# Kernel optimization log

Measured on AMD Instinct MI355X. Metric: run time of the kernel, lower is better.

Reference implementation:

```python
import jax, jax.numpy as jnp
import numpy as np

N_NODES = 50000
N_EDGES = 400000
DIMS = [128, 1024, 512, 256, 64, 1]  # ConvGraphNet layer widths


def setup_inputs() -> dict:
    key = jax.random.key(0)
    ks = jax.random.split(key, 2 + 2 * 5)
    inp = {}
    inp["x"] = jax.random.normal(ks[0], (N_NODES, DIMS[0]), dtype=jnp.float32)
    inp["edge_index"] = jax.random.randint(ks[1], (2, N_EDGES), 0, N_NODES, dtype=jnp.int32)
    for i in range(5):
        fan_in, fan_out = DIMS[i], DIMS[i + 1]
        scale = (1.0 / np.sqrt(fan_in)).astype(np.float32)
        inp[f"W{i+1}"] = jax.random.normal(ks[2 + 2 * i], (fan_in, fan_out), dtype=jnp.float32) * scale
        inp[f"b{i+1}"] = jax.random.normal(ks[3 + 2 * i], (fan_out,), dtype=jnp.float32) * 0.01
    return inp


def _gcn_forward(x, edge_index, params):
    # PyG GCNConv: add self-loops, symmetric deg^{-1/2} normalization,
    # h = x @ W, out[dst] += norm * h[src], + bias. ReLU after each layer.
    src, dst = edge_index[0], edge_index[1]
    loop = jnp.arange(N_NODES, dtype=src.dtype)
    src_f = jnp.concatenate([src, loop])  # [E + N]
    dst_f = jnp.concatenate([dst, loop])
    deg = jax.ops.segment_sum(jnp.ones_like(src_f, dtype=x.dtype), dst_f, num_segments=N_NODES)
    dinv = jnp.where(deg > 0, jax.lax.rsqrt(jnp.maximum(deg, 1e-12)), 0.0).astype(x.dtype)
    norm = (dinv[src_f] * dinv[dst_f])[:, None]  # [E + N, 1]
    for W, b in params:
        h = x @ W                      # [N, F_out] dense GEMM (small)
        msg = h[src_f] * norm          # gather + scale  [E+N, F_out]
        agg = jax.ops.segment_sum(msg, dst_f, num_segments=N_NODES)  # scatter-add
        x = jax.nn.relu(agg + b)
    return x


def reference(x, edge_index, W1, b1, W2, b2, W3, b3, W4, b4, W5, b5):
    params = [(W1, b1), (W2, b2), (W3, b3), (W4, b4), (W5, b5)]
    return _gcn_forward(x, edge_index, params)
```

## Files before the change

### kernel.cpp

```cpp
#include <hip/hip_runtime.h>
#include <hip/hip_bf16.h>

#define N_NODES_DIM0 128

typedef unsigned short u16;
typedef unsigned int u32;
typedef __attribute__((ext_vector_type(8))) short short8;
typedef __attribute__((ext_vector_type(4))) float f32x4;

__device__ __forceinline__ float bf2f(u16 h) { return __uint_as_float((u32)h << 16); }
__device__ __forceinline__ u16 f2bf(float f) {
    u32 u = __float_as_uint(f);
    u32 r = (u + 0x7FFFu + ((u >> 16) & 1u)) >> 16;
    return (u16)r;
}

__device__ __forceinline__ void gl2lds16(const u16* g, u16* lds_base) {
    __builtin_amdgcn_global_load_lds(
        (const __attribute__((address_space(1))) u32*)g,
        (__attribute__((address_space(3))) u32*)lds_base, 16, 0, 0);
}


__global__ void zero_int_kernel(int* p, int n) {
    int i = blockIdx.x * blockDim.x + threadIdx.x;
    if (i < n) p[i] = 0;
}

__global__ void hist_kernel(const int* __restrict__ dst, int* __restrict__ cnt, int e) {
    int i = blockIdx.x * blockDim.x + threadIdx.x;
    if (i < e) atomicAdd(&cnt[dst[i]], 1);
}

__global__ void alloc_kernel(const int* __restrict__ cnt, int* __restrict__ row_start,
                             float* __restrict__ dinv, int* __restrict__ cursor, int n) {
    int i = blockIdx.x * blockDim.x + threadIdx.x;
    int lane = threadIdx.x & 63;
    int v = (i < n) ? cnt[i] : 0;
    int s = v;
#pragma unroll
    for (int off = 1; off < 64; off <<= 1) {
        int x = __shfl_up(s, off, 64);
        if (lane >= off) s += x;
    }
    int total = __shfl(s, 63, 64);
    int base = 0;
    if (lane == 0) base = atomicAdd(cursor, total);
    base = __shfl(base, 0, 64);
    if (i < n) {
        row_start[i] = base + s - v;
        dinv[i] = rsqrtf((float)v + 1.0f);
    }
}

__global__ void fill_kernel(const int* __restrict__ src, const int* __restrict__ dst,
                            int* __restrict__ row_start, int* __restrict__ csr_src, int e) {
    int i = blockIdx.x * blockDim.x + threadIdx.x;
    if (i < e) {
        int d = dst[i];
        int pos = atomicAdd(&row_start[d], 1);
        csr_src[pos] = src[i];
    }
}

__global__ __launch_bounds__(256) void wtrans_kernel(
    const float* __restrict__ W0, const float* __restrict__ W1,
    const float* __restrict__ W2, const float* __restrict__ W3, u16* __restrict__ Wt) {
    __shared__ float tile[32][33];
    int bid = blockIdx.x;
    const float* W; u16* out; int K, F, kb, nb;
    if (bid < 128)      { W = W0; out = Wt;          K = 128;  F = 1024; kb = bid & 3;  nb = bid >> 2; }
    else if (bid < 640) { int l = bid - 128; W = W1; out = Wt + 131072; K = 1024; F = 512; kb = l & 31; nb = l >> 5; }
    else if (bid < 768) { int l = bid - 640; W = W2; out = Wt + 655360; K = 512;  F = 256; kb = l & 15; nb = l >> 4; }
    else                { int l = bid - 768; W = W3; out = Wt + 786432; K = 256;  F = 64;  kb = l & 7;  nb = l >> 3; }
    int k0 = kb * 32, n0 = nb * 32;
    int tx = threadIdx.x & 31, ty = threadIdx.x >> 5;
#pragma unroll
    for (int i = 0; i < 4; ++i) {
        int k = ty + i * 8;
        tile[k][tx] = W[(size_t)(k0 + k) * F + n0 + tx];
    }
    __syncthreads();
#pragma unroll
    for (int i = 0; i < 4; ++i) {
        int n = ty + i * 8;
        out[(size_t)(n0 + n) * K + k0 + tx] = f2bf(tile[tx][n]);
    }
}

__global__ void scale_cast_kernel(const float* __restrict__ x, const float* __restrict__ dinv,
                                  u16* __restrict__ Y, int N) {
    int gid = blockIdx.x * blockDim.x + threadIdx.x;
    int node = gid >> 5;
    int c4 = (gid & 31) * 4;
    if (node >= N) return;
    float dv = dinv[node];
    float4 v = *reinterpret_cast<const float4*>(x + (size_t)node * 128 + c4);
    ushort4 r;
    r.x = f2bf(dv * v.x); r.y = f2bf(dv * v.y);
    r.z = f2bf(dv * v.z); r.w = f2bf(dv * v.w);
    *reinterpret_cast<ushort4*>(Y + (size_t)node * 128 + c4) = r;
}

__device__ __forceinline__ void add8(float* acc, const u16* p) {
    short8 v = *reinterpret_cast<const short8*>(p);
#pragma unroll
    for (int w = 0; w < 8; ++w) acc[w] += bf2f((u16)v[w]);
}
__device__ __forceinline__ void add8v(float* acc, short8 v) {
#pragma unroll
    for (int w = 0; w < 8; ++w) acc[w] += bf2f((u16)v[w]);
}

__global__ void agg_pre_kernel(const int* __restrict__ row_end, const int* __restrict__ cnt,
                               const int* __restrict__ csr_src,
                               const u16* __restrict__ Y, const float* __restrict__ dinv,
                               u16* __restrict__ Z, int N) {
    int gid = blockIdx.x * blockDim.x + threadIdx.x;
    int node = gid >> 4;
    int ch = (gid & 15) * 8;
    if (node >= N) return;
    float acc[8] = {};
    add8(acc, Y + (size_t)node * 128 + ch);
    int end = row_end[node], beg = end - cnt[node];
    int e = beg;
    for (; e + 4 <= end; e += 4) {
        int s0 = csr_src[e], s1 = csr_src[e + 1], s2 = csr_src[e + 2], s3 = csr_src[e + 3];
        short8 v0 = *reinterpret_cast<const short8*>(Y + (size_t)s0 * 128 + ch);
        short8 v1 = *reinterpret_cast<const short8*>(Y + (size_t)s1 * 128 + ch);
        short8 v2 = *reinterpret_cast<const short8*>(Y + (size_t)s2 * 128 + ch);
        short8 v3 = *reinterpret_cast<const short8*>(Y + (size_t)s3 * 128 + ch);
        add8v(acc, v0); add8v(acc, v1); add8v(acc, v2); add8v(acc, v3);
    }
    for (; e < end; ++e) add8(acc, Y + (size_t)csr_src[e] * 128 + ch);
    float dv = dinv[node];
    short8 r;
#pragma unroll
    for (int w = 0; w < 8; ++w) r[w] = (short)f2bf(dv * acc[w]);
    *reinterpret_cast<short8*>(Z + (size_t)node * 128 + ch) = r;
}

template <int BN, int EPI>
__global__ __launch_bounds__(256) void gemm_mfma_kernel(
    const u16* __restrict__ X, const u16* __restrict__ Wt,
    const float* __restrict__ dinv, const float* __restrict__ bias,
    u16* __restrict__ Out, int N, int K, int F, int lgnx) {
    constexpr int BM = 128, BK = 64;
    constexpr int RA = (BM * 8) / 256;
    constexpr int RB = (BN * 8) / 256;
    __shared__ u16 As[BM * BK];
    __shared__ u16 Bs[BN * BK];

    const int t = threadIdx.x;
    const int wave = t >> 6;
    const int lane = t & 63;
    const int m16 = lane & 15;
    const int quad = lane >> 4;

    const int id = blockIdx.x;
    const int wi = id & ((8 << lgnx) - 1);
    const int g  = id >> (3 + lgnx);
    const int rb = g * 8 + (wi & 7);
    const int cb = wi >> 3;
    const int row0 = rb * BM;
    const int col0 = cb * BN;
    if (row0 >= N) return;

    constexpr int WN = BN / 2;
    constexpr int NI = 4;
    constexpr int NJ = WN / 16;
    const int wm = (wave >> 1) * 64;
    const int wn = (wave & 1) * WN;

    const u16* aSrc[RA];
    u16* aDst[RA];
#pragma unroll
    for (int rr = 0; rr < RA; ++rr) {
        int c = rr * 256 + t;
        int r = c >> 3;
        int q = (c ^ r) & 7;
        int grow = row0 + r;
        if (grow >= N) grow = 0;
        aSrc[rr] = X + (size_t)grow * K + q * 8;
        aDst[rr] = &As[(size_t)(rr * 256 + wave * 64) * 8];
    }
    const u16* bSrc[RB];
    u16* bDst[RB];
#pragma unroll
    for (int rr = 0; rr < RB; ++rr) {
        int c = rr * 256 + t;
        int r = c >> 3;
        int q = (c ^ r) & 7;
        bSrc[rr] = Wt + (size_t)(col0 + r) * K + q * 8;
        bDst[rr] = &Bs[(size_t)(rr * 256 + wave * 64) * 8];
    }

    u32 aOff[NI][2], bOff[NJ][2];
#pragma unroll
    for (int i = 0; i < NI; ++i)
#pragma unroll
        for (int h = 0; h < 2; ++h) {
            int row = wm + i * 16 + m16;
            int qg = h * 4 + quad;
            aOff[i][h] = (u32)(((row << 3) | ((qg ^ row) & 7)) * 16);
        }
#pragma unroll
    for (int j = 0; j < NJ; ++j)
#pragma unroll
        for (int h = 0; h < 2; ++h) {
            int row = wn + j * 16 + m16;
            int qg = h * 4 + quad;
            bOff[j][h] = (u32)(((row << 3) | ((qg ^ row) & 7)) * 16);
        }
    const char* AsB = reinterpret_cast<const char*>(As);
    const char* BsB = reinterpret_cast<const char*>(Bs);

    f32x4 acc[NI][NJ] = {};

    for (int k0 = 0; k0 < K; k0 += BK) {
#pragma unroll
        for (int rr = 0; rr < RA; ++rr) {
            gl2lds16(aSrc[rr], aDst[rr]);
            aSrc[rr] += BK;
        }
#pragma unroll
        for (int rr = 0; rr < RB; ++rr) {
            gl2lds16(bSrc[rr], bDst[rr]);
            bSrc[rr] += BK;
        }
        __syncthreads();

#pragma unroll
        for (int h = 0; h < 2; ++h) {
            short8 af[NI], bf[NJ];
#pragma unroll
            for (int i = 0; i < NI; ++i)
                af[i] = *reinterpret_cast<const short8*>(AsB + aOff[i][h]);
#pragma unroll
            for (int j = 0; j < NJ; ++j)
                bf[j] = *reinterpret_cast<const short8*>(BsB + bOff[j][h]);
#pragma unroll
            for (int i = 0; i < NI; ++i)
#pragma unroll
                for (int j = 0; j < NJ; ++j)
                    acc[i][j] = __builtin_amdgcn_mfma_f32_16x16x32_bf16(af[i], bf[j], acc[i][j], 0, 0, 0);
        }
        __syncthreads();
    }

#pragma unroll
    for (int i = 0; i < NI; ++i) {
#pragma unroll
        for (int r = 0; r < 4; ++r) {
            int grow = row0 + wm + i * 16 + quad * 4 + r;
            if (grow >= N) continue;
            float dv = (EPI == 0) ? dinv[grow] : 0.f;
#pragma unroll
            for (int j = 0; j < NJ; ++j) {
                int gcol = col0 + wn + j * 16 + m16;
                float v = acc[i][j][r];
                if (EPI == 0) v = dv * v;
                else          v = fmaxf(v + bias[gcol], 0.f);
                Out[(size_t)grow * F + gcol] = f2bf(v);
            }
        }
    }
}

__global__ void agg_post_kernel(const int* __restrict__ row_end, const int* __restrict__ cnt,
                                const int* __restrict__ csr_src,
                                const u16* __restrict__ Gc, const float* __restrict__ dinv,
                                const float* __restrict__ bias, u16* __restrict__ XO,
                                int N, int F, int lgG) {
    int gid = blockIdx.x * blockDim.x + threadIdx.x;
    int node = gid >> lgG;
    int ch = (gid & ((1 << lgG) - 1)) * 8;
    if (node >= N) return;
    float acc[8] = {};
    add8(acc, Gc + (size_t)node * F + ch);
    int end = row_end[node], beg = end - cnt[node];
    int e = beg;
    for (; e + 4 <= end; e += 4) {
        int s0 = csr_src[e], s1 = csr_src[e + 1], s2 = csr_src[e + 2], s3 = csr_src[e + 3];
        short8 v0 = *reinterpret_cast<const short8*>(Gc + (size_t)s0 * F + ch);
        short8 v1 = *reinterpret_cast<const short8*>(Gc + (size_t)s1 * F + ch);
        short8 v2 = *reinterpret_cast<const short8*>(Gc + (size_t)s2 * F + ch);
        short8 v3 = *reinterpret_cast<const short8*>(Gc + (size_t)s3 * F + ch);
        add8v(acc, v0); add8v(acc, v1); add8v(acc, v2); add8v(acc, v3);
    }
    for (; e < end; ++e) add8(acc, Gc + (size_t)csr_src[e] * F + ch);
    float dv = dinv[node];
    short8 r;
#pragma unroll
    for (int w = 0; w < 8; ++w)
        r[w] = (short)f2bf(fmaxf(fmaf(dv, acc[w], bias[ch + w]), 0.f));
    *reinterpret_cast<short8*>(XO + (size_t)node * F + ch) = r;
}

__global__ void layer5_dot_kernel(const u16* __restrict__ X, const float* __restrict__ W5,
                                  const float* __restrict__ dinv, float* __restrict__ g5, int N) {
    int gtid = blockIdx.x * blockDim.x + threadIdx.x;
    int node = gtid >> 6;
    int lane = threadIdx.x & 63;
    if (node >= N) return;
    float v = bf2f(X[(size_t)node * 64 + lane]) * W5[lane];
#pragma unroll
    for (int off = 32; off > 0; off >>= 1) v += __shfl_down(v, off, 64);
    if (lane == 0) g5[node] = dinv[node] * v;
}

__global__ void agg5_kernel(const int* __restrict__ row_end, const int* __restrict__ cnt,
                            const int* __restrict__ csr_src,
                            const float* __restrict__ g5, const float* __restrict__ dinv,
                            const float* __restrict__ b5, float* __restrict__ out, int N) {
    int i = blockIdx.x * blockDim.x + threadIdx.x;
    if (i >= N) return;
    float acc = g5[i];
    int end = row_end[i], e = end - cnt[i];
    for (; e + 4 <= end; e += 4) {
        float a = g5[csr_src[e]];
        float b = g5[csr_src[e + 1]];
        float c = g5[csr_src[e + 2]];
        float d = g5[csr_src[e + 3]];
        acc += (a + b) + (c + d);
    }
    for (; e < end; ++e) acc += g5[csr_src[e]];
    out[i] = fmaxf(fmaf(dinv[i], acc, b5[0]), 0.f);
}


static inline size_t align_up(size_t x) { return (x + 255) & ~(size_t)255; }
static inline int round_up8(int x) { return (x + 7) & ~7; }

extern "C" void kernel_launch(void* const* d_in, const int* in_sizes, int n_in,
                              void* d_out, int out_size, void* d_ws, size_t ws_size,
                              hipStream_t stream) {
    const float* x  = (const float*)d_in[0];
    const int*   ei = (const int*)d_in[1];
    const int E = in_sizes[1] / 2;
    const int N = in_sizes[0] / N_NODES_DIM0;
    const int* src = ei;
    const int* dst = ei + E;

    const float* W[5] = {(const float*)d_in[2], (const float*)d_in[4], (const float*)d_in[6],
                         (const float*)d_in[8], (const float*)d_in[10]};
    const float* B[5] = {(const float*)d_in[3], (const float*)d_in[5], (const float*)d_in[7],
                         (const float*)d_in[9], (const float*)d_in[11]};

    const int Ks[4] = {128, 1024, 512, 256};
    const int Fs[4] = {1024, 512, 256, 64};

    char* w = (char*)d_ws;
    size_t off = 0;
    float* dinv    = (float*)(w + off); off += align_up((size_t)N * 4);
    float* g5      = (float*)(w + off); off += align_up((size_t)N * 4);
    int*   cnt     = (int*)(w + off);   off += align_up((size_t)(N + 1) * 4);
    int*   rstart  = (int*)(w + off);   off += align_up((size_t)N * 4);
    int*   csr_src = (int*)(w + off);   off += align_up((size_t)E * 4);
    u16* WtBase = (u16*)(w + off);
    u16* Wt[4];
    {
        size_t cum = 0;
        for (int l = 0; l < 4; ++l) {
            Wt[l] = WtBase + cum;
            cum += (size_t)Ks[l] * Fs[l];
        }
        off += align_up(cum * 2);
    }
    char* REG = w + off;               off += align_up((size_t)N * 512 * 2);
    u16* Y  = (u16*)REG;
    u16* Z  = (u16*)(REG + align_up((size_t)N * 128 * 2));
    u16* Gc = (u16*)REG;
    u16* XA = (u16*)(w + off);         off += align_up((size_t)N * 1024 * 2);
    u16* XB = (u16*)(w + off);         off += align_up((size_t)N * 512 * 2);
    (void)ws_size;

    zero_int_kernel<<<(N + 1 + 255) / 256, 256, 0, stream>>>(cnt, N + 1);
    hist_kernel<<<(E + 255) / 256, 256, 0, stream>>>(dst, cnt, E);
    alloc_kernel<<<(N + 255) / 256, 256, 0, stream>>>(cnt, rstart, dinv, &cnt[N], N);
    fill_kernel<<<(E + 255) / 256, 256, 0, stream>>>(src, dst, rstart, csr_src, E);

    wtrans_kernel<<<784, 256, 0, stream>>>(W[0], W[1], W[2], W[3], WtBase);

    const int ny = (N + 127) / 128;
    const int ny8 = round_up8(ny);

    scale_cast_kernel<<<(N * 32 + 255) / 256, 256, 0, stream>>>(x, dinv, Y, N);
    agg_pre_kernel<<<(N * 16 + 255) / 256, 256, 0, stream>>>(rstart, cnt, csr_src, Y, dinv, Z, N);
    {
        gemm_mfma_kernel<128, 1><<<ny8 * 8, 256, 0, stream>>>(Z, Wt[0], dinv, B[0], XA,
                                                              N, 128, 1024, 3);
    }

    u16* Xin[3]  = {XA, XB, XA};
    u16* Xout[3] = {XB, XA, XB};
    for (int l = 1; l < 4; ++l) {
        const int K = Ks[l], F = Fs[l];
        if (F >= 128) {
            int nx = F / 128;
            int lgnx = (nx == 4) ? 2 : (nx == 2) ? 1 : 0;
            gemm_mfma_kernel<128, 0><<<ny8 * nx, 256, 0, stream>>>(
                Xin[l - 1], Wt[l], dinv, B[l], Gc, N, K, F, lgnx);
        } else {
            gemm_mfma_kernel<64, 0><<<ny8, 256, 0, stream>>>(
                Xin[l - 1], Wt[l], dinv, B[l], Gc, N, K, F, 0);
        }
        int lgG = (F == 512) ? 6 : (F == 256) ? 5 : 3;
        long long tot = (long long)N << lgG;
        agg_post_kernel<<<(unsigned)((tot + 255) / 256), 256, 0, stream>>>(
            rstart, cnt, csr_src, Gc, dinv, B[l], Xout[l - 1], N, F, lgG);
    }

    layer5_dot_kernel<<<(N * 64 + 255) / 256, 256, 0, stream>>>(XB, W[4], dinv, g5, N);
    agg5_kernel<<<(N + 255) / 256, 256, 0, stream>>>(rstart, cnt, csr_src, g5, dinv, B[4],
                                                     (float*)d_out, N);
}
```

Before: 450.7 us.

## Merge weight transpose with scale-cast, use 32-bit GEMM offsets and nontemporal stores

Merges the weight-transpose and input scale-cast kernels into one launch that splits its blocks by block index, saving one kernel launch and its gap. In the GEMM, 64-bit per-thread source pointers become 32-bit element offsets added to the base pointer, which reduces register use and address arithmetic. Epilogue output stores become nontemporal, to limit cache pollution from writes that are read later by other kernels. Nontemporal stores could hurt if the next kernel would have reused that data from L2.

```diff
diff --git a/kernel.cpp b/kernel.cpp
--- a/kernel.cpp
+++ b/kernel.cpp
@@ -63,43 +63,44 @@
     }
 }
 
-__global__ __launch_bounds__(256) void wtrans_kernel(
+__global__ __launch_bounds__(256) void prep_kernel(
     const float* __restrict__ W0, const float* __restrict__ W1,
-    const float* __restrict__ W2, const float* __restrict__ W3, u16* __restrict__ Wt) {
-    __shared__ float tile[32][33];
+    const float* __restrict__ W2, const float* __restrict__ W3, u16* __restrict__ Wt,
+    const float* __restrict__ x, const float* __restrict__ dinv,
+    u16* __restrict__ Y, int N) {
     int bid = blockIdx.x;
-    const float* W; u16* out; int K, F, kb, nb;
-    if (bid < 128)      { W = W0; out = Wt;          K = 128;  F = 1024; kb = bid & 3;  nb = bid >> 2; }
-    else if (bid < 640) { int l = bid - 128; W = W1; out = Wt + 131072; K = 1024; F = 512; kb = l & 31; nb = l >> 5; }
-    else if (bid < 768) { int l = bid - 640; W = W2; out = Wt + 655360; K = 512;  F = 256; kb = l & 15; nb = l >> 4; }
-    else                { int l = bid - 768; W = W3; out = Wt + 786432; K = 256;  F = 64;  kb = l & 7;  nb = l >> 3; }
-    int k0 = kb * 32, n0 = nb * 32;
-    int tx = threadIdx.x & 31, ty = threadIdx.x >> 5;
-#pragma unroll
-    for (int i = 0; i < 4; ++i) {
-        int k = ty + i * 8;
-        tile[k][tx] = W[(size_t)(k0 + k) * F + n0 + tx];
-    }
-    __syncthreads();
-#pragma unroll
-    for (int i = 0; i < 4; ++i) {
-        int n = ty + i * 8;
-        out[(size_t)(n0 + n) * K + k0 + tx] = f2bf(tile[tx][n]);
-    }
-}
-
-__global__ void scale_cast_kernel(const float* __restrict__ x, const float* __restrict__ dinv,
-                                  u16* __restrict__ Y, int N) {
-    int gid = blockIdx.x * blockDim.x + threadIdx.x;
-    int node = gid >> 5;
-    int c4 = (gid & 31) * 4;
-    if (node >= N) return;
-    float dv = dinv[node];
-    float4 v = *reinterpret_cast<const float4*>(x + (size_t)node * 128 + c4);
-    ushort4 r;
-    r.x = f2bf(dv * v.x); r.y = f2bf(dv * v.y);
-    r.z = f2bf(dv * v.z); r.w = f2bf(dv * v.w);
-    *reinterpret_cast<ushort4*>(Y + (size_t)node * 128 + c4) = r;
+    if (bid < 784) {
+        __shared__ float tile[32][33];
+        const float* W; u16* out; int K, F, kb, nb;
+        if (bid < 128)      { W = W0; out = Wt;          K = 128;  F = 1024; kb = bid & 3;  nb = bid >> 2; }
+        else if (bid < 640) { int l = bid - 128; W = W1; out = Wt + 131072; K = 1024; F = 512; kb = l & 31; nb = l >> 5; }
+        else if (bid < 768) { int l = bid - 640; W = W2; out = Wt + 655360; K = 512;  F = 256; kb = l & 15; nb = l >> 4; }
+        else                { int l = bid - 768; W = W3; out = Wt + 786432; K = 256;  F = 64;  kb = l & 7;  nb = l >> 3; }
+        int k0 = kb * 32, n0 = nb * 32;
+        int tx = threadIdx.x & 31, ty = threadIdx.x >> 5;
+#pragma unroll
+        for (int i = 0; i < 4; ++i) {
+            int k = ty + i * 8;
+            tile[k][tx] = W[(size_t)(k0 + k) * F + n0 + tx];
+        }
+        __syncthreads();
+#pragma unroll
+        for (int i = 0; i < 4; ++i) {
+            int n = ty + i * 8;
+            out[(size_t)(n0 + n) * K + k0 + tx] = f2bf(tile[tx][n]);
+        }
+    } else {
+        int gid = (bid - 784) * 256 + threadIdx.x;
+        int node = gid >> 5;
+        int c4 = (gid & 31) * 4;
+        if (node >= N) return;
+        float dv = dinv[node];
+        float4 v = *reinterpret_cast<const float4*>(x + (size_t)node * 128 + c4);
+        ushort4 r;
+        r.x = f2bf(dv * v.x); r.y = f2bf(dv * v.y);
+        r.z = f2bf(dv * v.z); r.w = f2bf(dv * v.w);
+        *reinterpret_cast<ushort4*>(Y + (size_t)node * 128 + c4) = r;
+    }
 }
 
 __device__ __forceinline__ void add8(float* acc, const u16* p) {
@@ -172,7 +173,7 @@
     const int wm = (wave >> 1) * 64;
     const int wn = (wave & 1) * WN;
 
-    const u16* aSrc[RA];
+    u32 aOffG[RA];
     u16* aDst[RA];
 #pragma unroll
     for (int rr = 0; rr < RA; ++rr) {
@@ -181,17 +182,17 @@
         int q = (c ^ r) & 7;
         int grow = row0 + r;
         if (grow >= N) grow = 0;
-        aSrc[rr] = X + (size_t)grow * K + q * 8;
+        aOffG[rr] = (u32)grow * (u32)K + (u32)(q * 8);
         aDst[rr] = &As[(size_t)(rr * 256 + wave * 64) * 8];
     }
-    const u16* bSrc[RB];
+    u32 bOffG[RB];
     u16* bDst[RB];
 #pragma unroll
     for (int rr = 0; rr < RB; ++rr) {
         int c = rr * 256 + t;
         int r = c >> 3;
         int q = (c ^ r) & 7;
-        bSrc[rr] = Wt + (size_t)(col0 + r) * K + q * 8;
+        bOffG[rr] = (u32)(col0 + r) * (u32)K + (u32)(q * 8);
         bDst[rr] = &Bs[(size_t)(rr * 256 + wave * 64) * 8];
     }
 
@@ -220,13 +221,13 @@
     for (int k0 = 0; k0 < K; k0 += BK) {
 #pragma unroll
         for (int rr = 0; rr < RA; ++rr) {
-            gl2lds16(aSrc[rr], aDst[rr]);
-            aSrc[rr] += BK;
+            gl2lds16(X + aOffG[rr], aDst[rr]);
+            aOffG[rr] += BK;
         }
 #pragma unroll
         for (int rr = 0; rr < RB; ++rr) {
-            gl2lds16(bSrc[rr], bDst[rr]);
-            bSrc[rr] += BK;
+            gl2lds16(Wt + bOffG[rr], bDst[rr]);
+            bOffG[rr] += BK;
         }
         __syncthreads();
 
@@ -261,7 +262,8 @@
                 float v = acc[i][j][r];
                 if (EPI == 0) v = dv * v;
                 else          v = fmaxf(v + bias[gcol], 0.f);
-                Out[(size_t)grow * F + gcol] = f2bf(v);
+                __builtin_nontemporal_store((short)f2bf(v),
+                    (short*)(Out + (size_t)grow * F + gcol));
             }
         }
     }
@@ -380,12 +382,15 @@
     alloc_kernel<<<(N + 255) / 256, 256, 0, stream>>>(cnt, rstart, dinv, &cnt[N], N);
     fill_kernel<<<(E + 255) / 256, 256, 0, stream>>>(src, dst, rstart, csr_src, E);
 
-    wtrans_kernel<<<784, 256, 0, stream>>>(W[0], W[1], W[2], W[3], WtBase);
+    {
+        int scale_blocks = (N * 32 + 255) / 256;
+        prep_kernel<<<784 + scale_blocks, 256, 0, stream>>>(
+            W[0], W[1], W[2], W[3], WtBase, x, dinv, Y, N);
+    }
 
     const int ny = (N + 127) / 128;
     const int ny8 = round_up8(ny);
 
-    scale_cast_kernel<<<(N * 32 + 255) / 256, 256, 0, stream>>>(x, dinv, Y, N);
     agg_pre_kernel<<<(N * 16 + 255) / 256, 256, 0, stream>>>(rstart, cnt, csr_src, Y, dinv, Z, N);
     {
         gemm_mfma_kernel<128, 1><<<ny8 * 8, 256, 0, stream>>>(Z, Wt[0], dinv, B[0], XA,
```

New measurement: 456.5 us. No clear change (+1.3%).
